# Kernel tuning notes

Measured on AMD Instinct MI355X. Metric: run time of the kernel, lower is better.

Reference implementation:

```python
import jax, jax.numpy as jnp
import numpy as np

N_PROBLEMS = 20000
N_SKILLS = 1000
EMB_SIZE = 128
TIME_LOG = 5.0
B, L = 64, 1024


def setup_inputs() -> dict:
    key = jax.random.key(0)
    ks = jax.random.split(key, 10)
    skills = jax.random.randint(ks[0], (B, L), 0, N_SKILLS)
    problems = jax.random.randint(ks[1], (B, L), 0, N_PROBLEMS)
    labels = jax.random.randint(ks[2], (B, L), 0, 2)
    times = jnp.sort(jax.random.randint(ks[3], (B, L), 0, 1_000_000), axis=-1)
    inp = jnp.stack([skills, problems, labels, times], axis=1)  # [B,4,L]
    std = 0.01
    return {
        "input": inp,
        "problem_base": std * jax.random.normal(ks[4], (N_PROBLEMS, 1), jnp.float32),
        "skill_base": std * jax.random.normal(ks[5], (N_SKILLS, 1), jnp.float32),
        "alpha_inter": std * jax.random.normal(ks[6], (N_SKILLS * 2, EMB_SIZE), jnp.float32),
        "alpha_skill": std * jax.random.normal(ks[7], (N_SKILLS, EMB_SIZE), jnp.float32),
        "beta_inter": std * jax.random.normal(ks[8], (N_SKILLS * 2, EMB_SIZE), jnp.float32),
        "beta_skill": std * jax.random.normal(ks[9], (N_SKILLS, EMB_SIZE), jnp.float32),
    }


def reference(input, problem_base, skill_base, alpha_inter, alpha_skill, beta_inter, beta_skill):
    skills = input[:, 0]    # [B,L]
    problems = input[:, 1]
    labels = input[:, 2]
    times = input[:, 3]

    mask_labels = labels * (labels < 2).astype(labels.dtype)
    inters = skills + mask_labels * N_SKILLS  # [B,L] in [0, 2*N_SKILLS)

    # pairwise Hawkes excitation / decay scores: [B,L,L]
    alphas = jnp.einsum('bie,bje->bij', alpha_inter[inters], alpha_skill[skills])
    betas = jnp.einsum('bie,bje->bij', beta_inter[inters], beta_skill[skills])
    betas = jnp.clip(betas + 1.0, 0.0, 10.0)

    dt = jnp.abs(times[:, :, None] - times[:, None, :]).astype(jnp.float32)
    log_dt = jnp.log(dt + 1e-10) / np.log(TIME_LOG)

    cross_effects = alphas * jnp.exp(-betas * log_dt)

    seq_len = skills.shape[1]
    # keep strictly-upper-triangular entries (source i before target j)
    keep = jnp.triu(jnp.ones((seq_len, seq_len), dtype=bool), k=1)
    sum_t = jnp.where(keep[None], cross_effects, 0.0).sum(axis=-2)  # [B,L]

    problem_bias = problem_base[problems][..., 0]
    skill_bias = skill_base[skills][..., 0]
    return jax.nn.sigmoid(problem_bias + skill_bias + sum_t)
```

## Files before the change

### kernel.cpp

```cpp
#include <hip/hip_runtime.h>
#include <hip/hip_bf16.h>

#define NB   64
#define SL   1024
#define EMB  128
#define NSK  1000
#define TI   64
#define SB   136
#define NS   2

#define AI_OFF 0
#define BI_OFF 256000
#define AS_OFF 512000
#define BS_OFF 640000
#define TB_ELEMS 768000
#define ACC_BYTE_OFF (TB_ELEMS * 2)

using short8  = __attribute__((ext_vector_type(8))) short;
using floatx4 = __attribute__((ext_vector_type(4))) float;

#define INV_LOG2_5 0.43067655807339306f

__device__ inline unsigned cvt2(float x, float y) {
    float2 f; f.x = x; f.y = y;
    __hip_bfloat162 h = __float22bfloat162_rn(f);
    unsigned u; __builtin_memcpy(&u, &h, sizeof(u));
    return u;
}

extern "C" __global__ __launch_bounds__(256)
void cvt_tables(const float* __restrict__ ai, const float* __restrict__ bi,
                const float* __restrict__ as, const float* __restrict__ bs,
                unsigned short* __restrict__ dst)
{
    const int t = blockIdx.x * 256 + threadIdx.x;
    const long e = (long)t * 8;
    const float* src;
    if      (e < 256000) src = ai + e;
    else if (e < 512000) src = bi + (e - 256000);
    else if (e < 640000) src = as + (e - 512000);
    else                 src = bs + (e - 640000);
    float4 f0 = *(const float4*)src;
    float4 f1 = *(const float4*)(src + 4);
    uint4 pk;
    pk.x = cvt2(f0.x, f0.y); pk.y = cvt2(f0.z, f0.w);
    pk.z = cvt2(f1.x, f1.y); pk.w = cvt2(f1.z, f1.w);
    *(uint4*)(dst + e) = pk;
}

__device__ float fixup_pair(const float* __restrict__ air,
                            const float* __restrict__ bir,
                            const float* __restrict__ asr,
                            const float* __restrict__ bsr) {
    float da = 0.f, db = 0.f;
    for (int k = 0; k < EMB; ++k) {
        da += air[k] * asr[k];
        db += bir[k] * bsr[k];
    }
    float beta = fminf(fmaxf(db + 1.f, 0.f), 10.f);
    return da * __expf(beta * 14.30676558073393f);
}

extern "C" __global__ __launch_bounds__(256, 4)
void hawkes_main(const int*   __restrict__ inp,
                 const unsigned short* __restrict__ tb,
                 float*       __restrict__ acc)
{
    __shared__ unsigned short lA[2][TI][SB];

    const int bid  = blockIdx.x;
    const int b    = bid & (NB - 1);
    const int r    = bid >> 6;
    const int jt   = 15 - (r >> 1);
    const int s    = r & 1;
    const int tid  = threadIdx.x;
    const int w    = tid >> 6;
    const int l    = tid & 63;
    const int quad = l >> 4;
    const int col  = l & 15;

    const int* __restrict__ binp = inp + b * 4 * SL;

    const int jlane = jt * TI + w * 16 + col;
    const int sk_j  = binp[jlane];
    const int tj    = binp[3 * SL + jlane];

    const unsigned short* asr16 = tb + AS_OFF + (long)sk_j * EMB + quad * 8;
    const unsigned short* bsr16 = tb + BS_OFF + (long)sk_j * EMB + quad * 8;
    short8 bfa[4], bfb[4];
#pragma unroll
    for (int ks = 0; ks < 4; ++ks) {
        bfa[ks] = *(const short8*)(asr16 + ks * 32);
        bfb[ks] = *(const short8*)(bsr16 + ks * 32);
    }

    const int srow = tid >> 2;
    const int sq   = tid & 3;
    unsigned short* dA = &lA[0][srow][sq * 32];
    unsigned short* dB = &lA[1][srow][sq * 32];

    float sum = 0.f;

    if (s <= jt) {
        uint4 pa0, pa1, pa2, pa3, pb0, pb1, pb2, pb3;
        {
            const int irow  = s * TI + srow;
            const int ski   = binp[irow];
            const int li    = binp[2 * SL + irow];
            const long intr = ski + (long)li * NSK;
            const unsigned short* sA  = tb + AI_OFF + intr * EMB + sq * 32;
            const unsigned short* sBm = tb + BI_OFF + intr * EMB + sq * 32;
            pa0 = *(const uint4*)(sA);      pa1 = *(const uint4*)(sA + 8);
            pa2 = *(const uint4*)(sA + 16); pa3 = *(const uint4*)(sA + 24);
            pb0 = *(const uint4*)(sBm);     pb1 = *(const uint4*)(sBm + 8);
            pb2 = *(const uint4*)(sBm + 16);pb3 = *(const uint4*)(sBm + 24);
        }

        for (int it = s; it <= jt; it += NS) {
            __syncthreads();
            *(uint4*)(dA)      = pa0; *(uint4*)(dA + 8)  = pa1;
            *(uint4*)(dA + 16) = pa2; *(uint4*)(dA + 24) = pa3;
            *(uint4*)(dB)      = pb0; *(uint4*)(dB + 8)  = pb1;
            *(uint4*)(dB + 16) = pb2; *(uint4*)(dB + 24) = pb3;

            if (it + NS <= jt) {
                const int irow  = (it + NS) * TI + srow;
                const int ski   = binp[irow];
                const int li    = binp[2 * SL + irow];
                const long intr = ski + (long)li * NSK;
                const unsigned short* sA  = tb + AI_OFF + intr * EMB + sq * 32;
                const unsigned short* sBm = tb + BI_OFF + intr * EMB + sq * 32;
                pa0 = *(const uint4*)(sA);      pa1 = *(const uint4*)(sA + 8);
                pa2 = *(const uint4*)(sA + 16); pa3 = *(const uint4*)(sA + 24);
                pb0 = *(const uint4*)(sBm);     pb1 = *(const uint4*)(sBm + 8);
                pb2 = *(const uint4*)(sBm + 16);pb3 = *(const uint4*)(sBm + 24);
            }
            __syncthreads();

            const int itb = it * TI;
#pragma unroll
            for (int isub = 0; isub < 4; ++isub) {
                floatx4 aa = {0.f, 0.f, 0.f, 0.f};
                floatx4 bb = {0.f, 0.f, 0.f, 0.f};
#pragma unroll
                for (int ks = 0; ks < 4; ++ks) {
                    const int k0 = ks * 32 + quad * 8;
                    short8 av = *(const short8*)&lA[0][isub * 16 + col][k0];
                    short8 bv = *(const short8*)&lA[1][isub * 16 + col][k0];
                    aa = __builtin_amdgcn_mfma_f32_16x16x32_bf16(av, bfa[ks], aa, 0, 0, 0);
                    bb = __builtin_amdgcn_mfma_f32_16x16x32_bf16(bv, bfb[ks], bb, 0, 0, 0);
                }
                const int ibase = itb + isub * 16 + quad * 4;
                const int4 t4 = *(const int4*)(binp + 3 * SL + ibase);
#pragma unroll
                for (int rr = 0; rr < 4; ++rr) {
                    const int ti = (rr == 0) ? t4.x : (rr == 1) ? t4.y : (rr == 2) ? t4.z : t4.w;
                    const int dt = tj - ti;
                    float lc  = __log2f((float)dt);
                    float nb  = fminf(fmaxf(bb[rr] + 1.f, 0.f), 10.f) * (-INV_LOG2_5);
                    float arg = (dt > 0) ? nb * lc : -__builtin_inff();
                    sum += aa[rr] * exp2f(arg);
                }
            }
        }
    }

    sum += __shfl_xor(sum, 16, 64);
    sum += __shfl_xor(sum, 32, 64);

    if (quad == 0) {
        acc[(((long)s * NB + b) << 10) + jlane] = sum;
    }
}

extern "C" __global__ __launch_bounds__(256)
void hawkes_finalize(const int* __restrict__ inp, const float* __restrict__ pbase,
                     const float* __restrict__ sbase,
                     const float* __restrict__ ai, const float* __restrict__ as,
                     const float* __restrict__ bi, const float* __restrict__ bs,
                     const float* __restrict__ acc, float* __restrict__ out)
{
    const int t = blockIdx.x * 256 + threadIdx.x;
    const int b = t >> 10, j = t & (SL - 1);
    const int* binp = inp + b * 4 * SL;
    const int tj   = binp[3 * SL + j];
    const int sk_j = binp[j];

    float corr = 0.f;
    for (int i = j - 1; i >= 0 && binp[3 * SL + i] == tj; --i) {
        const int ski = binp[i], li = binp[2 * SL + i];
        const long intr = ski + (long)li * NSK;
        corr += fixup_pair(ai + intr * EMB, bi + intr * EMB,
                           as + (long)sk_j * EMB, bs + (long)sk_j * EMB);
    }

    float sum = acc[t] + acc[NB * SL + t] + corr;
    const float x = pbase[binp[SL + j]] + sbase[sk_j] + sum;
    out[t] = 1.f / (1.f + __expf(-x));
}

extern "C" void kernel_launch(void* const* d_in, const int* in_sizes, int n_in,
                              void* d_out, int out_size, void* d_ws, size_t ws_size,
                              hipStream_t stream) {
    const int*   inp = (const int*)d_in[0];
    const float* pb  = (const float*)d_in[1];
    const float* sb  = (const float*)d_in[2];
    const float* ai  = (const float*)d_in[3];
    const float* as  = (const float*)d_in[4];
    const float* bi  = (const float*)d_in[5];
    const float* bs  = (const float*)d_in[6];

    unsigned short* tb  = (unsigned short*)d_ws;
    float*          acc = (float*)((char*)d_ws + ACC_BYTE_OFF);

    cvt_tables<<<dim3(96000 / 256), dim3(256), 0, stream>>>(ai, bi, as, bs, tb);
    hawkes_main<<<dim3(NB * 16 * NS), dim3(256), 0, stream>>>(inp, tb, acc);
    hawkes_finalize<<<dim3(NB * SL / 256), dim3(256), 0, stream>>>(
        inp, pb, sb, ai, as, bi, bs, acc, (float*)d_out);
}
```

Before: 115.1 us.

## Widen j-tile to 128 with XOR-swizzled LDS and four-way i-split

```diff
diff --git a/kernel.cpp b/kernel.cpp
--- a/kernel.cpp
+++ b/kernel.cpp
@@ -5,9 +5,7 @@
 #define SL   1024
 #define EMB  128
 #define NSK  1000
-#define TI   64
-#define SB   136
-#define NS   2
+#define NS   4
 
 #define AI_OFF 0
 #define BI_OFF 256000
@@ -66,13 +64,13 @@
                  const unsigned short* __restrict__ tb,
                  float*       __restrict__ acc)
 {
-    __shared__ unsigned short lA[2][TI][SB];
+    __shared__ unsigned short lA[2][64][128];
 
     const int bid  = blockIdx.x;
     const int b    = bid & (NB - 1);
     const int r    = bid >> 6;
-    const int jt   = 15 - (r >> 1);
-    const int s    = r & 1;
+    const int jt   = 7 - (r >> 2);
+    const int s    = r & 3;
     const int tid  = threadIdx.x;
     const int w    = tid >> 6;
     const int l    = tid & 63;
@@ -81,30 +79,39 @@
 
     const int* __restrict__ binp = inp + b * 4 * SL;
 
-    const int jlane = jt * TI + w * 16 + col;
-    const int sk_j  = binp[jlane];
-    const int tj    = binp[3 * SL + jlane];
-
-    const unsigned short* asr16 = tb + AS_OFF + (long)sk_j * EMB + quad * 8;
-    const unsigned short* bsr16 = tb + BS_OFF + (long)sk_j * EMB + quad * 8;
-    short8 bfa[4], bfb[4];
-#pragma unroll
-    for (int ks = 0; ks < 4; ++ks) {
-        bfa[ks] = *(const short8*)(asr16 + ks * 32);
-        bfb[ks] = *(const short8*)(bsr16 + ks * 32);
+    const int j0 = jt * 128 + w * 16 + col;
+    const int j1 = j0 + 64;
+    const int sk0 = binp[j0],          sk1 = binp[j1];
+    const int tj0 = binp[3 * SL + j0], tj1 = binp[3 * SL + j1];
+
+    short8 bfa0[4], bfb0[4], bfa1[4], bfb1[4];
+    {
+        const unsigned short* p0a = tb + AS_OFF + (long)sk0 * EMB + quad * 8;
+        const unsigned short* p0b = tb + BS_OFF + (long)sk0 * EMB + quad * 8;
+        const unsigned short* p1a = tb + AS_OFF + (long)sk1 * EMB + quad * 8;
+        const unsigned short* p1b = tb + BS_OFF + (long)sk1 * EMB + quad * 8;
+#pragma unroll
+        for (int ks = 0; ks < 4; ++ks) {
+            bfa0[ks] = *(const short8*)(p0a + ks * 32);
+            bfb0[ks] = *(const short8*)(p0b + ks * 32);
+            bfa1[ks] = *(const short8*)(p1a + ks * 32);
+            bfb1[ks] = *(const short8*)(p1b + ks * 32);
+        }
     }
 
     const int srow = tid >> 2;
     const int sq   = tid & 3;
-    unsigned short* dA = &lA[0][srow][sq * 32];
-    unsigned short* dB = &lA[1][srow][sq * 32];
-
-    float sum = 0.f;
-
-    if (s <= jt) {
+    const int sw   = srow & 15;
+    unsigned short* rowA = &lA[0][srow][0];
+    unsigned short* rowB = &lA[1][srow][0];
+
+    float sum0 = 0.f, sum1 = 0.f;
+    const int itmax = 2 * jt + 1;
+
+    if (s <= itmax) {
         uint4 pa0, pa1, pa2, pa3, pb0, pb1, pb2, pb3;
         {
-            const int irow  = s * TI + srow;
+            const int irow  = s * 64 + srow;
             const int ski   = binp[irow];
             const int li    = binp[2 * SL + irow];
             const long intr = ski + (long)li * NSK;
@@ -116,15 +123,19 @@
             pb2 = *(const uint4*)(sBm + 16);pb3 = *(const uint4*)(sBm + 24);
         }
 
-        for (int it = s; it <= jt; it += NS) {
+        for (int it = s; it <= itmax; it += NS) {
             __syncthreads();
-            *(uint4*)(dA)      = pa0; *(uint4*)(dA + 8)  = pa1;
-            *(uint4*)(dA + 16) = pa2; *(uint4*)(dA + 24) = pa3;
-            *(uint4*)(dB)      = pb0; *(uint4*)(dB + 8)  = pb1;
-            *(uint4*)(dB + 16) = pb2; *(uint4*)(dB + 24) = pb3;
-
-            if (it + NS <= jt) {
-                const int irow  = (it + NS) * TI + srow;
+            *(uint4*)(rowA + (((sq * 4 + 0) ^ sw) * 8)) = pa0;
+            *(uint4*)(rowA + (((sq * 4 + 1) ^ sw) * 8)) = pa1;
+            *(uint4*)(rowA + (((sq * 4 + 2) ^ sw) * 8)) = pa2;
+            *(uint4*)(rowA + (((sq * 4 + 3) ^ sw) * 8)) = pa3;
+            *(uint4*)(rowB + (((sq * 4 + 0) ^ sw) * 8)) = pb0;
+            *(uint4*)(rowB + (((sq * 4 + 1) ^ sw) * 8)) = pb1;
+            *(uint4*)(rowB + (((sq * 4 + 2) ^ sw) * 8)) = pb2;
+            *(uint4*)(rowB + (((sq * 4 + 3) ^ sw) * 8)) = pb3;
+
+            if (it + NS <= itmax) {
+                const int irow  = (it + NS) * 64 + srow;
                 const int ski   = binp[irow];
                 const int li    = binp[2 * SL + irow];
                 const long intr = ski + (long)li * NSK;
@@ -137,39 +148,54 @@
             }
             __syncthreads();
 
-            const int itb = it * TI;
+            const int itb = it * 64;
 #pragma unroll
             for (int isub = 0; isub < 4; ++isub) {
-                floatx4 aa = {0.f, 0.f, 0.f, 0.f};
-                floatx4 bb = {0.f, 0.f, 0.f, 0.f};
+                floatx4 aa0 = {0.f,0.f,0.f,0.f}, bb0 = {0.f,0.f,0.f,0.f};
+                floatx4 aa1 = {0.f,0.f,0.f,0.f}, bb1 = {0.f,0.f,0.f,0.f};
+                const unsigned short* rrow0 = &lA[0][isub * 16 + col][0];
+                const unsigned short* rrow1 = &lA[1][isub * 16 + col][0];
 #pragma unroll
                 for (int ks = 0; ks < 4; ++ks) {
-                    const int k0 = ks * 32 + quad * 8;
-                    short8 av = *(const short8*)&lA[0][isub * 16 + col][k0];
-                    short8 bv = *(const short8*)&lA[1][isub * 16 + col][k0];
-                    aa = __builtin_amdgcn_mfma_f32_16x16x32_bf16(av, bfa[ks], aa, 0, 0, 0);
-                    bb = __builtin_amdgcn_mfma_f32_16x16x32_bf16(bv, bfb[ks], bb, 0, 0, 0);
+                    const int pc = ((ks * 4 + quad) ^ col) * 8;
+                    short8 av = *(const short8*)(rrow0 + pc);
+                    short8 bv = *(const short8*)(rrow1 + pc);
+                    aa0 = __builtin_amdgcn_mfma_f32_16x16x32_bf16(av, bfa0[ks], aa0, 0, 0, 0);
+                    aa1 = __builtin_amdgcn_mfma_f32_16x16x32_bf16(av, bfa1[ks], aa1, 0, 0, 0);
+                    bb0 = __builtin_amdgcn_mfma_f32_16x16x32_bf16(bv, bfb0[ks], bb0, 0, 0, 0);
+                    bb1 = __builtin_amdgcn_mfma_f32_16x16x32_bf16(bv, bfb1[ks], bb1, 0, 0, 0);
                 }
                 const int ibase = itb + isub * 16 + quad * 4;
                 const int4 t4 = *(const int4*)(binp + 3 * SL + ibase);
 #pragma unroll
                 for (int rr = 0; rr < 4; ++rr) {
                     const int ti = (rr == 0) ? t4.x : (rr == 1) ? t4.y : (rr == 2) ? t4.z : t4.w;
-                    const int dt = tj - ti;
-                    float lc  = __log2f((float)dt);
-                    float nb  = fminf(fmaxf(bb[rr] + 1.f, 0.f), 10.f) * (-INV_LOG2_5);
-                    float arg = (dt > 0) ? nb * lc : -__builtin_inff();
-                    sum += aa[rr] * exp2f(arg);
+                    {
+                        const int dt = tj0 - ti;
+                        float lc  = __log2f((float)dt);
+                        float nb  = fminf(fmaxf(bb0[rr] + 1.f, 0.f), 10.f) * (-INV_LOG2_5);
+                        float arg = (dt > 0) ? nb * lc : -__builtin_inff();
+                        sum0 += aa0[rr] * exp2f(arg);
+                    }
+                    {
+                        const int dt = tj1 - ti;
+                        float lc  = __log2f((float)dt);
+                        float nb  = fminf(fmaxf(bb1[rr] + 1.f, 0.f), 10.f) * (-INV_LOG2_5);
+                        float arg = (dt > 0) ? nb * lc : -__builtin_inff();
+                        sum1 += aa1[rr] * exp2f(arg);
+                    }
                 }
             }
         }
     }
 
-    sum += __shfl_xor(sum, 16, 64);
-    sum += __shfl_xor(sum, 32, 64);
+    sum0 += __shfl_xor(sum0, 16, 64); sum0 += __shfl_xor(sum0, 32, 64);
+    sum1 += __shfl_xor(sum1, 16, 64); sum1 += __shfl_xor(sum1, 32, 64);
 
     if (quad == 0) {
-        acc[(((long)s * NB + b) << 10) + jlane] = sum;
+        float* as_ = acc + (((long)s * NB + b) << 10);
+        as_[j0] = sum0;
+        as_[j1] = sum1;
     }
 }
 
@@ -194,7 +220,7 @@
                            as + (long)sk_j * EMB, bs + (long)sk_j * EMB);
     }
 
-    float sum = acc[t] + acc[NB * SL + t] + corr;
+    float sum = acc[t] + acc[NB * SL + t] + acc[2 * NB * SL + t] + acc[3 * NB * SL + t] + corr;
     const float x = pbase[binp[SL + j]] + sbase[sk_j] + sum;
     out[t] = 1.f / (1.f + __expf(-x));
 }
@@ -214,7 +240,7 @@
     float*          acc = (float*)((char*)d_ws + ACC_BYTE_OFF);
 
     cvt_tables<<<dim3(96000 / 256), dim3(256), 0, stream>>>(ai, bi, as, bs, tb);
-    hawkes_main<<<dim3(NB * 16 * NS), dim3(256), 0, stream>>>(inp, tb, acc);
+    hawkes_main<<<dim3(NB * 8 * NS), dim3(256), 0, stream>>>(inp, tb, acc);
     hawkes_finalize<<<dim3(NB * SL / 256), dim3(256), 0, stream>>>(
         inp, pb, sb, ai, as, bi, bs, acc, (float*)d_out);
 }
```

Measured after the change: 254.8 us. 121% more time.
